# Performance work log

Measured on AMD Instinct MI355X. Metric: run time of the kernel, lower is better.

The kernel has to match this reference:

```python
import jax, jax.numpy as jnp
import numpy as np

S, B, H, I, E = 512, 2, 1024, 2816, 8  # seq_len, batch, hidden, intermediate, num_local_experts


def setup_inputs() -> dict:
    key = jax.random.key(0)
    ks = jax.random.split(key, 5)
    return {
        "hidden_states": jax.random.normal(ks[0], (S, B, H), dtype=jnp.float32),
        "router_w": jax.random.normal(ks[1], (E, H), dtype=jnp.float32) * 0.02,
        "gate_w": jax.random.normal(ks[2], (E, I, H), dtype=jnp.float32) * 0.02,
        "up_w": jax.random.normal(ks[3], (E, I, H), dtype=jnp.float32) * 0.02,
        "down_w": jax.random.normal(ks[4], (E, H, I), dtype=jnp.float32) * 0.02,
    }


def reference(hidden_states, router_w, gate_w, up_w, down_w):
    # Router: linear hidden -> num_experts, top-1 routing (num_experts_per_tok == 1).
    router_logits = jnp.einsum('sbh,eh->sbe', hidden_states, router_w)  # [S,B,E]
    routing_indices = jnp.argmax(router_logits, axis=-1)  # [S,B], top-1 == argmax
    # NOTE: the source computes routing_weights = sigmoid(top logit) but never
    # applies it in _combine_expert_outputs; we faithfully omit the scaling.

    out = jnp.zeros_like(hidden_states)
    for e in range(E):  # fixed small expert count; masked dense dispatch/combine
        mask = (routing_indices == e)[..., None]  # [S,B,1]
        xe = jnp.where(mask, hidden_states, 0.0)
        g = jnp.einsum('sbh,ih->sbi', xe, gate_w[e])
        u = jnp.einsum('sbh,ih->sbi', xe, up_w[e])
        ye = jnp.einsum('sbi,hi->sbh', jax.nn.silu(g) * u, down_w[e])
        out = out + jnp.where(mask, ye, 0.0)
    return out
```

## Files before the change

kernel.cpp:

```cpp
#include <hip/hip_runtime.h>
#include <math.h>

constexpr int H_ = 1024;
constexpr int I_ = 2816;
constexpr int E_ = 8;
constexpr int T_ = 1024;

typedef __bf16 bf16x8 __attribute__((ext_vector_type(8)));
typedef float f32x4 __attribute__((ext_vector_type(4)));

__device__ __forceinline__ ushort f2bf(float f) {
    uint32_t u = __float_as_uint(f);
    u += 0x7fff + ((u >> 16) & 1);
    return (ushort)(u >> 16);
}
__device__ __forceinline__ uint pack2(float lo, float hi) {
    return (uint)f2bf(lo) | ((uint)f2bf(hi) << 16);
}
__device__ __forceinline__ bf16x8 cvt8(float4 a, float4 b) {
    union { uint u[4]; bf16x8 v; } r;
    r.u[0] = pack2(a.x, a.y); r.u[1] = pack2(a.z, a.w);
    r.u[2] = pack2(b.x, b.y); r.u[3] = pack2(b.z, b.w);
    return r.v;
}
__device__ __forceinline__ bf16x8 as_bf16x8(uint4 v) {
    union { uint4 u; bf16x8 b; } c; c.u = v; return c.b;
}


__global__ __launch_bounds__(64) void router_kernel(const float* __restrict__ hidden,
                                                    const float* __restrict__ rw,
                                                    int* __restrict__ counts,
                                                    int* __restrict__ tlist,
                                                    ushort* __restrict__ xbf) {
    const int t = blockIdx.x;
    const int lane = threadIdx.x;
    const float* x = hidden + (size_t)t * H_ + lane * 16;
    float4 v[4];
#pragma unroll
    for (int j = 0; j < 4; j++) v[j] = ((const float4*)x)[j];
    uint2* xb = (uint2*)(xbf + (size_t)t * H_ + lane * 16);
#pragma unroll
    for (int j = 0; j < 4; j++) xb[j] = make_uint2(pack2(v[j].x, v[j].y), pack2(v[j].z, v[j].w));
    float acc[E_];
#pragma unroll
    for (int e = 0; e < E_; e++) {
        const float4* r = (const float4*)(rw + e * H_ + lane * 16);
        float a = 0.f;
#pragma unroll
        for (int j = 0; j < 4; j++) {
            float4 rv = r[j];
            a += v[j].x * rv.x + v[j].y * rv.y + v[j].z * rv.z + v[j].w * rv.w;
        }
        acc[e] = a;
    }
#pragma unroll
    for (int e = 0; e < E_; e++) {
#pragma unroll
        for (int off = 32; off >= 1; off >>= 1)
            acc[e] += __shfl_xor(acc[e], off, 64);
    }
    if (lane == 0) {
        int best = 0;
        float bv = acc[0];
#pragma unroll
        for (int e = 1; e < E_; e++) {
            if (acc[e] > bv) { bv = acc[e]; best = e; }
        }
        int pos = atomicAdd(&counts[best], 1);
        tlist[best * T_ + pos] = t;
    }
}

__global__ __launch_bounds__(256, 2) void gateup_kernel(const ushort* __restrict__ xbf,
                                                        const float* __restrict__ gate_w,
                                                        const float* __restrict__ up_w,
                                                        const int* __restrict__ counts,
                                                        const int* __restrict__ tlist,
                                                        ushort* __restrict__ act) {
    const int e  = blockIdx.y;
    const int i0 = blockIdx.x * 32;
    const int cnt = counts[e];
    const int tid = threadIdx.x;
    const int wv = tid >> 6, lane = tid & 63, quad = lane >> 4, l15 = lane & 15;

    __shared__ int toks[256];

    const float* gw0 = gate_w + ((size_t)e * I_ + i0 + l15) * H_ + quad * 8;
    const float* gw1 = gw0 + (size_t)16 * H_;
    const float* uw0 = up_w   + ((size_t)e * I_ + i0 + l15) * H_ + quad * 8;
    const float* uw1 = uw0 + (size_t)16 * H_;

    for (int toff = 0; toff < cnt; toff += 256) {
        __syncthreads();
        { int p = toff + tid; toks[tid] = (p < cnt) ? tlist[e * T_ + p] : -1; }
        __syncthreads();
        if (cnt - toff <= wv * 64) continue;

        int tka[4];
        const ushort* xa[4];
#pragma unroll
        for (int mi = 0; mi < 4; mi++) {
            tka[mi] = toks[wv * 64 + mi * 16 + l15];
            xa[mi] = xbf + (size_t)(tka[mi] < 0 ? 0 : tka[mi]) * H_ + quad * 8;
        }

        f32x4 accg[4][2], accu[4][2];
#pragma unroll
        for (int mi = 0; mi < 4; mi++)
#pragma unroll
            for (int nj = 0; nj < 2; nj++) {
                accg[mi][nj] = (f32x4){0.f, 0.f, 0.f, 0.f};
                accu[mi][nj] = (f32x4){0.f, 0.f, 0.f, 0.f};
            }

        uint4 a0[4], a1[4];
        float4 g0[2][2], g1[2][2], u0[2][2], u1[2][2];

#define GU_LOAD(A, G, U, kk) do {                                                   \
        const int k_ = (kk);                                                        \
        _Pragma("unroll")                                                           \
        for (int mi = 0; mi < 4; mi++)                                              \
            A[mi] = (tka[mi] >= 0) ? *(const uint4*)(xa[mi] + k_)                   \
                                   : make_uint4(0u, 0u, 0u, 0u);                    \
        G[0][0] = *(const float4*)(gw0 + k_); G[0][1] = *(const float4*)(gw0 + k_ + 4); \
        G[1][0] = *(const float4*)(gw1 + k_); G[1][1] = *(const float4*)(gw1 + k_ + 4); \
        U[0][0] = *(const float4*)(uw0 + k_); U[0][1] = *(const float4*)(uw0 + k_ + 4); \
        U[1][0] = *(const float4*)(uw1 + k_); U[1][1] = *(const float4*)(uw1 + k_ + 4); \
    } while (0)

#define GU_MFMA(A, G, U) do {                                                       \
        bf16x8 bg[2], bu[2];                                                        \
        _Pragma("unroll")                                                           \
        for (int nj = 0; nj < 2; nj++) {                                            \
            bg[nj] = cvt8(G[nj][0], G[nj][1]);                                      \
            bu[nj] = cvt8(U[nj][0], U[nj][1]);                                      \
        }                                                                           \
        _Pragma("unroll")                                                           \
        for (int mi = 0; mi < 4; mi++) {                                            \
            bf16x8 aa = as_bf16x8(A[mi]);                                           \
            _Pragma("unroll")                                                       \
            for (int nj = 0; nj < 2; nj++) {                                        \
                accg[mi][nj] = __builtin_amdgcn_mfma_f32_16x16x32_bf16(aa, bg[nj], accg[mi][nj], 0, 0, 0); \
                accu[mi][nj] = __builtin_amdgcn_mfma_f32_16x16x32_bf16(aa, bu[nj], accu[mi][nj], 0, 0, 0); \
            }                                                                       \
        }                                                                           \
    } while (0)

        GU_LOAD(a0, g0, u0, 0);
#pragma unroll 1
        for (int k0 = 0; k0 < H_; k0 += 64) {
            GU_LOAD(a1, g1, u1, k0 + 32);
            GU_MFMA(a0, g0, u0);
            if (k0 + 64 < H_) GU_LOAD(a0, g0, u0, k0 + 64);
            GU_MFMA(a1, g1, u1);
        }
#undef GU_LOAD
#undef GU_MFMA

#pragma unroll
        for (int mi = 0; mi < 4; mi++)
#pragma unroll
            for (int r = 0; r < 4; r++) {
                int tok = toks[wv * 64 + mi * 16 + quad * 4 + r];
                if (tok < 0) continue;
#pragma unroll
                for (int nj = 0; nj < 2; nj++) {
                    float g = accg[mi][nj][r], u = accu[mi][nj][r];
                    float s = g / (1.f + __expf(-g)) * u;
                    act[(size_t)tok * I_ + i0 + nj * 16 + l15] = f2bf(s);
                }
            }
    }
}

__global__ __launch_bounds__(256, 2) void down_kernel(const ushort* __restrict__ act,
                                                      const float* __restrict__ down_w,
                                                      const int* __restrict__ counts,
                                                      const int* __restrict__ tlist,
                                                      float* __restrict__ out) {
    const int e  = blockIdx.y;
    const int h0 = blockIdx.x * 16;
    const int cnt = counts[e];
    const int tid = threadIdx.x;
    const int wv = tid >> 6, lane = tid & 63, quad = lane >> 4, l15 = lane & 15;

    __shared__ int toks[256];
    const float* dw = down_w + ((size_t)e * H_ + h0 + l15) * I_ + quad * 8;

    for (int toff = 0; toff < cnt; toff += 256) {
        __syncthreads();
        { int p = toff + tid; toks[tid] = (p < cnt) ? tlist[e * T_ + p] : -1; }
        __syncthreads();
        if (cnt - toff <= wv * 64) continue;

        int tka[4];
        const ushort* xa[4];
#pragma unroll
        for (int mi = 0; mi < 4; mi++) {
            tka[mi] = toks[wv * 64 + mi * 16 + l15];
            xa[mi] = act + (size_t)(tka[mi] < 0 ? 0 : tka[mi]) * I_ + quad * 8;
        }

        f32x4 acc[4];
#pragma unroll
        for (int mi = 0; mi < 4; mi++) acc[mi] = (f32x4){0.f, 0.f, 0.f, 0.f};

        uint4 a0[4], a1[4];
        float4 d0[2], d1[2];

#define DN_LOAD(A, D, kk) do {                                                      \
        const int k_ = (kk);                                                        \
        _Pragma("unroll")                                                           \
        for (int mi = 0; mi < 4; mi++)                                              \
            A[mi] = (tka[mi] >= 0) ? *(const uint4*)(xa[mi] + k_)                   \
                                   : make_uint4(0u, 0u, 0u, 0u);                    \
        D[0] = *(const float4*)(dw + k_); D[1] = *(const float4*)(dw + k_ + 4);     \
    } while (0)

#define DN_MFMA(A, D) do {                                                          \
        bf16x8 bd = cvt8(D[0], D[1]);                                               \
        _Pragma("unroll")                                                           \
        for (int mi = 0; mi < 4; mi++) {                                            \
            bf16x8 aa = as_bf16x8(A[mi]);                                           \
            acc[mi] = __builtin_amdgcn_mfma_f32_16x16x32_bf16(aa, bd, acc[mi], 0, 0, 0); \
        }                                                                           \
    } while (0)

        DN_LOAD(a0, d0, 0);
#pragma unroll 1
        for (int k0 = 0; k0 < I_; k0 += 64) {
            DN_LOAD(a1, d1, k0 + 32);
            DN_MFMA(a0, d0);
            if (k0 + 64 < I_) DN_LOAD(a0, d0, k0 + 64);
            DN_MFMA(a1, d1);
        }
#undef DN_LOAD
#undef DN_MFMA

#pragma unroll
        for (int mi = 0; mi < 4; mi++)
#pragma unroll
            for (int r = 0; r < 4; r++) {
                int tok = toks[wv * 64 + mi * 16 + quad * 4 + r];
                if (tok < 0) continue;
                out[(size_t)tok * H_ + h0 + l15] = acc[mi][r];
            }
    }
}

extern "C" void kernel_launch(void* const* d_in, const int* in_sizes, int n_in,
                              void* d_out, int out_size, void* d_ws, size_t ws_size,
                              hipStream_t stream) {
    const float* hidden = (const float*)d_in[0];
    const float* rw     = (const float*)d_in[1];
    const float* gate_w = (const float*)d_in[2];
    const float* up_w   = (const float*)d_in[3];
    const float* down_w = (const float*)d_in[4];
    float* out = (float*)d_out;

    int* counts = (int*)d_ws;
    int* tlist  = counts + E_;
    ushort* xbf = (ushort*)(tlist + E_ * T_);
    ushort* act = xbf + (size_t)T_ * H_;

    hipMemsetAsync(counts, 0, E_ * sizeof(int), stream);
    hipLaunchKernelGGL(router_kernel, dim3(T_), dim3(64), 0, stream, hidden, rw, counts, tlist, xbf);
    hipLaunchKernelGGL(gateup_kernel, dim3(I_ / 32, E_), dim3(256), 0, stream,
                       xbf, gate_w, up_w, counts, tlist, act);
    hipLaunchKernelGGL(down_kernel, dim3(H_ / 16, E_), dim3(256), 0, stream,
                       act, down_w, counts, tlist, out);
}
```

Baseline: 423.1 us.

## Stage gate/up and down operands through LDS with async global-to-LDS copies

Both the gate/up and down kernels now stream activations and weights into swizzled shared memory using global_load_lds async copies. The gate/up kernel double-buffers and the down kernel triple-buffers, with manual vmcnt waits and barriers in place of per-wave register prefetch from global memory. The fp32 weight tile is loaded once per block and shared across the four waves instead of each wave loading it separately, and gateup occupancy is raised to 3 blocks. The cost is extra LDS use, a barrier on every k-step, and hand-tuned wait counts that must match the number of issued copies. Waves with no tokens no longer skip the main loop, so they do redundant work.

```diff
diff --git a/kernel.cpp b/kernel.cpp
--- a/kernel.cpp
+++ b/kernel.cpp
@@ -23,8 +23,23 @@
     r.u[2] = pack2(b.x, b.y); r.u[3] = pack2(b.z, b.w);
     return r.v;
 }
-__device__ __forceinline__ bf16x8 as_bf16x8(uint4 v) {
-    union { uint4 u; bf16x8 b; } c; c.u = v; return c.b;
+
+__device__ __forceinline__ void async_copy16(void* lds, const void* g) {
+    __builtin_amdgcn_global_load_lds(
+        (const __attribute__((address_space(1))) void*)g,
+        (__attribute__((address_space(3))) void*)lds, 16, 0, 0);
+}
+
+__device__ __forceinline__ bf16x8 ldsA(const ushort* base, int row, int quad) {
+    int bir = (quad * 16) ^ (((row >> 1) & 3) << 4);
+    return *(const bf16x8*)((const char*)base + row * 64 + bir);
+}
+__device__ __forceinline__ bf16x8 ldsB(const float* base, int row, int quad) {
+    int sw = (row & 7) << 4;
+    const char* r = (const char*)base + row * 128;
+    float4 x = *(const float4*)(r + ((quad * 32) ^ sw));
+    float4 y = *(const float4*)(r + ((quad * 32 + 16) ^ sw));
+    return cvt8(x, y);
 }
 
 
@@ -72,7 +87,7 @@
     }
 }
 
-__global__ __launch_bounds__(256, 2) void gateup_kernel(const ushort* __restrict__ xbf,
+__global__ __launch_bounds__(256, 3) void gateup_kernel(const ushort* __restrict__ xbf,
                                                         const float* __restrict__ gate_w,
                                                         const float* __restrict__ up_w,
                                                         const int* __restrict__ counts,
@@ -84,25 +99,29 @@
     const int tid = threadIdx.x;
     const int wv = tid >> 6, lane = tid & 63, quad = lane >> 4, l15 = lane & 15;
 
+    __shared__ ushort Xs[2 * 256 * 32];
+    __shared__ float  Gs[2 * 32 * 32];
+    __shared__ float  Us[2 * 32 * 32];
     __shared__ int toks[256];
 
-    const float* gw0 = gate_w + ((size_t)e * I_ + i0 + l15) * H_ + quad * 8;
-    const float* gw1 = gw0 + (size_t)16 * H_;
-    const float* uw0 = up_w   + ((size_t)e * I_ + i0 + l15) * H_ + quad * 8;
-    const float* uw1 = uw0 + (size_t)16 * H_;
+    const int wrow = tid >> 3;
+    const int wbir = ((tid & 7) << 4) ^ ((wrow & 7) << 4);
+    const float* gsrc = gate_w + ((size_t)e * I_ + i0 + wrow) * H_ + (wbir >> 2);
+    const float* usrc = up_w   + ((size_t)e * I_ + i0 + wrow) * H_ + (wbir >> 2);
 
     for (int toff = 0; toff < cnt; toff += 256) {
         __syncthreads();
         { int p = toff + tid; toks[tid] = (p < cnt) ? tlist[e * T_ + p] : -1; }
         __syncthreads();
-        if (cnt - toff <= wv * 64) continue;
-
-        int tka[4];
-        const ushort* xa[4];
-#pragma unroll
-        for (int mi = 0; mi < 4; mi++) {
-            tka[mi] = toks[wv * 64 + mi * 16 + l15];
-            xa[mi] = xbf + (size_t)(tka[mi] < 0 ? 0 : tka[mi]) * H_ + quad * 8;
+
+        const ushort* xsrc[4];
+#pragma unroll
+        for (int p = 0; p < 4; p++) {
+            int row = p * 64 + (tid >> 2);
+            int tok = toks[row];
+            if (tok < 0) tok = 0;
+            int birl = ((tid & 3) << 4) ^ (((row >> 1) & 3) << 4);
+            xsrc[p] = xbf + (size_t)tok * H_ + (birl >> 1);
         }
 
         f32x4 accg[4][2], accu[4][2];
@@ -114,49 +133,53 @@
                 accu[mi][nj] = (f32x4){0.f, 0.f, 0.f, 0.f};
             }
 
-        uint4 a0[4], a1[4];
-        float4 g0[2][2], g1[2][2], u0[2][2], u1[2][2];
-
-#define GU_LOAD(A, G, U, kk) do {                                                   \
-        const int k_ = (kk);                                                        \
-        _Pragma("unroll")                                                           \
-        for (int mi = 0; mi < 4; mi++)                                              \
-            A[mi] = (tka[mi] >= 0) ? *(const uint4*)(xa[mi] + k_)                   \
-                                   : make_uint4(0u, 0u, 0u, 0u);                    \
-        G[0][0] = *(const float4*)(gw0 + k_); G[0][1] = *(const float4*)(gw0 + k_ + 4); \
-        G[1][0] = *(const float4*)(gw1 + k_); G[1][1] = *(const float4*)(gw1 + k_ + 4); \
-        U[0][0] = *(const float4*)(uw0 + k_); U[0][1] = *(const float4*)(uw0 + k_ + 4); \
-        U[1][0] = *(const float4*)(uw1 + k_); U[1][1] = *(const float4*)(uw1 + k_ + 4); \
+#define GSTAGE(buf, kofs) do {                                                  \
+        char* xb_ = (char*)Xs + (buf) * 16384 + wv * 1024;                      \
+        _Pragma("unroll")                                                       \
+        for (int p = 0; p < 4; p++)                                             \
+            async_copy16(xb_ + p * 4096, xsrc[p] + (kofs));                     \
+        async_copy16((char*)Gs + (buf) * 4096 + wv * 1024, gsrc + (kofs));      \
+        async_copy16((char*)Us + (buf) * 4096 + wv * 1024, usrc + (kofs));      \
     } while (0)
 
-#define GU_MFMA(A, G, U) do {                                                       \
-        bf16x8 bg[2], bu[2];                                                        \
-        _Pragma("unroll")                                                           \
-        for (int nj = 0; nj < 2; nj++) {                                            \
-            bg[nj] = cvt8(G[nj][0], G[nj][1]);                                      \
-            bu[nj] = cvt8(U[nj][0], U[nj][1]);                                      \
-        }                                                                           \
-        _Pragma("unroll")                                                           \
-        for (int mi = 0; mi < 4; mi++) {                                            \
-            bf16x8 aa = as_bf16x8(A[mi]);                                           \
-            _Pragma("unroll")                                                       \
-            for (int nj = 0; nj < 2; nj++) {                                        \
-                accg[mi][nj] = __builtin_amdgcn_mfma_f32_16x16x32_bf16(aa, bg[nj], accg[mi][nj], 0, 0, 0); \
-                accu[mi][nj] = __builtin_amdgcn_mfma_f32_16x16x32_bf16(aa, bu[nj], accu[mi][nj], 0, 0, 0); \
-            }                                                                       \
-        }                                                                           \
-    } while (0)
-
-        GU_LOAD(a0, g0, u0, 0);
+        GSTAGE(0, 0);
+        int cur = 0;
 #pragma unroll 1
-        for (int k0 = 0; k0 < H_; k0 += 64) {
-            GU_LOAD(a1, g1, u1, k0 + 32);
-            GU_MFMA(a0, g0, u0);
-            if (k0 + 64 < H_) GU_LOAD(a0, g0, u0, k0 + 64);
-            GU_MFMA(a1, g1, u1);
-        }
-#undef GU_LOAD
-#undef GU_MFMA
+        for (int k0 = 0; k0 < H_; k0 += 32) {
+            if (k0 + 32 < H_) {
+                GSTAGE(cur ^ 1, k0 + 32);
+                asm volatile("s_waitcnt vmcnt(6)" ::: "memory");
+            } else {
+                asm volatile("s_waitcnt vmcnt(0)" ::: "memory");
+            }
+            __builtin_amdgcn_s_barrier();
+            __builtin_amdgcn_sched_barrier(0);
+
+            const ushort* Xb = Xs + cur * 8192;
+            const float*  Gb = Gs + cur * 1024;
+            const float*  Ub = Us + cur * 1024;
+            bf16x8 a[4], bg[2], bu[2];
+#pragma unroll
+            for (int nj = 0; nj < 2; nj++) {
+                bg[nj] = ldsB(Gb, nj * 16 + l15, quad);
+                bu[nj] = ldsB(Ub, nj * 16 + l15, quad);
+            }
+#pragma unroll
+            for (int mi = 0; mi < 4; mi++)
+                a[mi] = ldsA(Xb, wv * 64 + mi * 16 + l15, quad);
+#pragma unroll
+            for (int mi = 0; mi < 4; mi++)
+#pragma unroll
+                for (int nj = 0; nj < 2; nj++) {
+                    accg[mi][nj] = __builtin_amdgcn_mfma_f32_16x16x32_bf16(a[mi], bg[nj], accg[mi][nj], 0, 0, 0);
+                    accu[mi][nj] = __builtin_amdgcn_mfma_f32_16x16x32_bf16(a[mi], bu[nj], accu[mi][nj], 0, 0, 0);
+                }
+            __builtin_amdgcn_sched_barrier(0);
+            __builtin_amdgcn_s_barrier();
+            __builtin_amdgcn_sched_barrier(0);
+            cur ^= 1;
+        }
+#undef GSTAGE
 
 #pragma unroll
         for (int mi = 0; mi < 4; mi++)
@@ -185,58 +208,78 @@
     const int tid = threadIdx.x;
     const int wv = tid >> 6, lane = tid & 63, quad = lane >> 4, l15 = lane & 15;
 
+    __shared__ ushort As[3 * 256 * 32];
+    __shared__ float  Ds[3 * 16 * 32];
     __shared__ int toks[256];
-    const float* dw = down_w + ((size_t)e * H_ + h0 + l15) * I_ + quad * 8;
+
+    const int wrow = (tid >> 3) & 15;
+    const int wbir = ((tid & 7) << 4) ^ ((wrow & 7) << 4);
+    const float* dsrc = down_w + ((size_t)e * H_ + h0 + wrow) * I_ + (wbir >> 2);
 
     for (int toff = 0; toff < cnt; toff += 256) {
         __syncthreads();
         { int p = toff + tid; toks[tid] = (p < cnt) ? tlist[e * T_ + p] : -1; }
         __syncthreads();
-        if (cnt - toff <= wv * 64) continue;
-
-        int tka[4];
-        const ushort* xa[4];
-#pragma unroll
-        for (int mi = 0; mi < 4; mi++) {
-            tka[mi] = toks[wv * 64 + mi * 16 + l15];
-            xa[mi] = act + (size_t)(tka[mi] < 0 ? 0 : tka[mi]) * I_ + quad * 8;
+
+        const ushort* asrc[4];
+#pragma unroll
+        for (int p = 0; p < 4; p++) {
+            int row = p * 64 + (tid >> 2);
+            int tok = toks[row];
+            if (tok < 0) tok = 0;
+            int birl = ((tid & 3) << 4) ^ (((row >> 1) & 3) << 4);
+            asrc[p] = act + (size_t)tok * I_ + (birl >> 1);
         }
 
         f32x4 acc[4];
 #pragma unroll
         for (int mi = 0; mi < 4; mi++) acc[mi] = (f32x4){0.f, 0.f, 0.f, 0.f};
 
-        uint4 a0[4], a1[4];
-        float4 d0[2], d1[2];
-
-#define DN_LOAD(A, D, kk) do {                                                      \
-        const int k_ = (kk);                                                        \
-        _Pragma("unroll")                                                           \
-        for (int mi = 0; mi < 4; mi++)                                              \
-            A[mi] = (tka[mi] >= 0) ? *(const uint4*)(xa[mi] + k_)                   \
-                                   : make_uint4(0u, 0u, 0u, 0u);                    \
-        D[0] = *(const float4*)(dw + k_); D[1] = *(const float4*)(dw + k_ + 4);     \
+#define DSTAGE(buf, kofs) do {                                                  \
+        char* ab_ = (char*)As + (buf) * 16384 + wv * 1024;                      \
+        _Pragma("unroll")                                                       \
+        for (int p = 0; p < 4; p++)                                             \
+            async_copy16(ab_ + p * 4096, asrc[p] + (kofs));                     \
+        if (wv < 2)                                                             \
+            async_copy16((char*)Ds + (buf) * 2048 + wv * 1024, dsrc + (kofs));  \
     } while (0)
 
-#define DN_MFMA(A, D) do {                                                          \
-        bf16x8 bd = cvt8(D[0], D[1]);                                               \
-        _Pragma("unroll")                                                           \
-        for (int mi = 0; mi < 4; mi++) {                                            \
-            bf16x8 aa = as_bf16x8(A[mi]);                                           \
-            acc[mi] = __builtin_amdgcn_mfma_f32_16x16x32_bf16(aa, bd, acc[mi], 0, 0, 0); \
-        }                                                                           \
-    } while (0)
-
-        DN_LOAD(a0, d0, 0);
+        DSTAGE(0, 0);
+        DSTAGE(1, 32);
+        int cur = 0;
 #pragma unroll 1
-        for (int k0 = 0; k0 < I_; k0 += 64) {
-            DN_LOAD(a1, d1, k0 + 32);
-            DN_MFMA(a0, d0);
-            if (k0 + 64 < I_) DN_LOAD(a0, d0, k0 + 64);
-            DN_MFMA(a1, d1);
-        }
-#undef DN_LOAD
-#undef DN_MFMA
+        for (int k0 = 0; k0 < I_; k0 += 32) {
+            if (k0 + 64 < I_) {
+                int stg = cur ? cur - 1 : 2;
+                DSTAGE(stg, k0 + 64);
+                if (wv < 2) asm volatile("s_waitcnt vmcnt(10)" ::: "memory");
+                else        asm volatile("s_waitcnt vmcnt(8)"  ::: "memory");
+            } else if (k0 + 32 < I_) {
+                if (wv < 2) asm volatile("s_waitcnt vmcnt(5)" ::: "memory");
+                else        asm volatile("s_waitcnt vmcnt(4)" ::: "memory");
+            } else {
+                asm volatile("s_waitcnt vmcnt(0)" ::: "memory");
+            }
+            __builtin_amdgcn_s_barrier();
+            __builtin_amdgcn_sched_barrier(0);
+
+            const ushort* Ab = As + cur * 8192;
+            const float*  Db = Ds + cur * 512;
+            bf16x8 a[4];
+            bf16x8 bd = ldsB(Db, l15, quad);
+#pragma unroll
+            for (int mi = 0; mi < 4; mi++)
+                a[mi] = ldsA(Ab, wv * 64 + mi * 16 + l15, quad);
+#pragma unroll
+            for (int mi = 0; mi < 4; mi++)
+                acc[mi] = __builtin_amdgcn_mfma_f32_16x16x32_bf16(a[mi], bd, acc[mi], 0, 0, 0);
+
+            __builtin_amdgcn_sched_barrier(0);
+            __builtin_amdgcn_s_barrier();
+            __builtin_amdgcn_sched_barrier(0);
+            cur = (cur == 2) ? 0 : cur + 1;
+        }
+#undef DSTAGE
 
 #pragma unroll
         for (int mi = 0; mi < 4; mi++)
```

Measured after the change: 382.9 us. 1.1x faster.

## Stage expert weights into LDS with async global_load_lds and swizzled multi-buffering

Applied to the files above, without the earlier changes.

Both expert GEMM kernels now stream fp32 weight tiles into a 4-deep swizzled LDS ring using global_load_lds, with manual vmcnt waits and barriers. Previously each wave loaded the weights straight into registers. Sharing the staged tiles across the four waves removes redundant global weight loads, and the XOR swizzle avoids LDS bank conflicts. The patch also switches to the hardware packed bf16 convert, interleaves experts across a 1D grid, and raises gateup occupancy to 3. The tradeoffs are hand-tuned waitcnt counts that are fragile and the removal of early exit for idle waves, since all waves must now join the barriers.

```diff
diff --git a/kernel.cpp b/kernel.cpp
--- a/kernel.cpp
+++ b/kernel.cpp
@@ -17,14 +17,22 @@
 __device__ __forceinline__ uint pack2(float lo, float hi) {
     return (uint)f2bf(lo) | ((uint)f2bf(hi) << 16);
 }
-__device__ __forceinline__ bf16x8 cvt8(float4 a, float4 b) {
-    union { uint u[4]; bf16x8 v; } r;
-    r.u[0] = pack2(a.x, a.y); r.u[1] = pack2(a.z, a.w);
-    r.u[2] = pack2(b.x, b.y); r.u[3] = pack2(b.z, b.w);
-    return r.v;
-}
 __device__ __forceinline__ bf16x8 as_bf16x8(uint4 v) {
     union { uint4 u; bf16x8 b; } c; c.u = v; return c.b;
+}
+__device__ __forceinline__ bf16x8 cvt8pk(float4 a, float4 b) {
+    union { uint u[4]; bf16x8 v; } r;
+    asm("v_cvt_pk_bf16_f32 %0, %1, %2" : "=v"(r.u[0]) : "v"(a.x), "v"(a.y));
+    asm("v_cvt_pk_bf16_f32 %0, %1, %2" : "=v"(r.u[1]) : "v"(a.z), "v"(a.w));
+    asm("v_cvt_pk_bf16_f32 %0, %1, %2" : "=v"(r.u[2]) : "v"(b.x), "v"(b.y));
+    asm("v_cvt_pk_bf16_f32 %0, %1, %2" : "=v"(r.u[3]) : "v"(b.z), "v"(b.w));
+    return r.v;
+}
+
+__device__ __forceinline__ void async_copy16(void* lds, const void* g) {
+    __builtin_amdgcn_global_load_lds(
+        (const __attribute__((address_space(1))) void*)g,
+        (__attribute__((address_space(3))) void*)lds, 16, 0, 0);
 }
 
 
@@ -72,33 +80,41 @@
     }
 }
 
-__global__ __launch_bounds__(256, 2) void gateup_kernel(const ushort* __restrict__ xbf,
+__global__ __launch_bounds__(256, 3) void gateup_kernel(const ushort* __restrict__ xbf,
                                                         const float* __restrict__ gate_w,
                                                         const float* __restrict__ up_w,
                                                         const int* __restrict__ counts,
                                                         const int* __restrict__ tlist,
                                                         ushort* __restrict__ act) {
-    const int e  = blockIdx.y;
-    const int i0 = blockIdx.x * 32;
+    const int id = blockIdx.x;
+    const int e  = id & 7;
+    const int i0 = (id >> 3) * 32;
     const int cnt = counts[e];
     const int tid = threadIdx.x;
     const int wv = tid >> 6, lane = tid & 63, quad = lane >> 4, l15 = lane & 15;
 
+    __shared__ float Gs[4 * 1024];
+    __shared__ float Us[4 * 1024];
     __shared__ int toks[256];
 
-    const float* gw0 = gate_w + ((size_t)e * I_ + i0 + l15) * H_ + quad * 8;
-    const float* gw1 = gw0 + (size_t)16 * H_;
-    const float* uw0 = up_w   + ((size_t)e * I_ + i0 + l15) * H_ + quad * 8;
-    const float* uw1 = uw0 + (size_t)16 * H_;
+    const int wrow = tid >> 3;
+    const int wcol = (((tid & 7) ^ (wrow & 7)) << 2);
+    const float* gsrc = gate_w + ((size_t)e * I_ + i0 + wrow) * H_ + wcol;
+    const float* usrc = up_w   + ((size_t)e * I_ + i0 + wrow) * H_ + wcol;
+    char* gdst = (char*)Gs + wv * 1024;
+    char* udst = (char*)Us + wv * 1024;
+
+#define STAGEW(buf, kofs) do {                                                  \
+        async_copy16(gdst + (buf) * 4096, gsrc + (kofs));                       \
+        async_copy16(udst + (buf) * 4096, usrc + (kofs));                       \
+    } while (0)
 
     for (int toff = 0; toff < cnt; toff += 256) {
         __syncthreads();
         { int p = toff + tid; toks[tid] = (p < cnt) ? tlist[e * T_ + p] : -1; }
         __syncthreads();
-        if (cnt - toff <= wv * 64) continue;
-
-        int tka[4];
-        const ushort* xa[4];
+
+        int tka[4]; const ushort* xa[4];
 #pragma unroll
         for (int mi = 0; mi < 4; mi++) {
             tka[mi] = toks[wv * 64 + mi * 16 + l15];
@@ -114,49 +130,60 @@
                 accu[mi][nj] = (f32x4){0.f, 0.f, 0.f, 0.f};
             }
 
-        uint4 a0[4], a1[4];
-        float4 g0[2][2], g1[2][2], u0[2][2], u1[2][2];
-
-#define GU_LOAD(A, G, U, kk) do {                                                   \
-        const int k_ = (kk);                                                        \
-        _Pragma("unroll")                                                           \
-        for (int mi = 0; mi < 4; mi++)                                              \
-            A[mi] = (tka[mi] >= 0) ? *(const uint4*)(xa[mi] + k_)                   \
-                                   : make_uint4(0u, 0u, 0u, 0u);                    \
-        G[0][0] = *(const float4*)(gw0 + k_); G[0][1] = *(const float4*)(gw0 + k_ + 4); \
-        G[1][0] = *(const float4*)(gw1 + k_); G[1][1] = *(const float4*)(gw1 + k_ + 4); \
-        U[0][0] = *(const float4*)(uw0 + k_); U[0][1] = *(const float4*)(uw0 + k_ + 4); \
-        U[1][0] = *(const float4*)(uw1 + k_); U[1][1] = *(const float4*)(uw1 + k_ + 4); \
-    } while (0)
-
-#define GU_MFMA(A, G, U) do {                                                       \
-        bf16x8 bg[2], bu[2];                                                        \
-        _Pragma("unroll")                                                           \
-        for (int nj = 0; nj < 2; nj++) {                                            \
-            bg[nj] = cvt8(G[nj][0], G[nj][1]);                                      \
-            bu[nj] = cvt8(U[nj][0], U[nj][1]);                                      \
-        }                                                                           \
-        _Pragma("unroll")                                                           \
-        for (int mi = 0; mi < 4; mi++) {                                            \
-            bf16x8 aa = as_bf16x8(A[mi]);                                           \
-            _Pragma("unroll")                                                       \
-            for (int nj = 0; nj < 2; nj++) {                                        \
+        uint4 xc[4], xn[4];
+        STAGEW(0, 0);
+        STAGEW(1, 32);
+#pragma unroll
+        for (int mi = 0; mi < 4; mi++) xc[mi] = *(const uint4*)(xa[mi]);
+
+#define GBODY(k, XU, XL) do {                                                   \
+        const int t_ = (k) >> 5;                                                \
+        if ((k) + 32 < H_) {                                                    \
+            _Pragma("unroll")                                                   \
+            for (int mi = 0; mi < 4; mi++)                                      \
+                XL[mi] = *(const uint4*)(xa[mi] + (k) + 32);                    \
+        }                                                                       \
+        __builtin_amdgcn_sched_barrier(0);                                      \
+        if ((k) + 64 < H_) {                                                    \
+            STAGEW((t_ + 2) & 3, (k) + 64);                                     \
+            __builtin_amdgcn_sched_barrier(0);                                  \
+            asm volatile("s_waitcnt vmcnt(12)" ::: "memory");                   \
+        } else {                                                                \
+            asm volatile("s_waitcnt vmcnt(0)" ::: "memory");                    \
+        }                                                                       \
+        __builtin_amdgcn_s_barrier();                                           \
+        __builtin_amdgcn_sched_barrier(0);                                      \
+        const float* Gb = Gs + (t_ & 3) * 1024;                                 \
+        const float* Ub = Us + (t_ & 3) * 1024;                                 \
+        bf16x8 bg[2], bu[2];                                                    \
+        const int sw_ = (l15 & 7) << 4;                                         \
+        _Pragma("unroll")                                                       \
+        for (int nj = 0; nj < 2; nj++) {                                        \
+            const char* gr = (const char*)Gb + (nj * 16 + l15) * 128;           \
+            const char* ur = (const char*)Ub + (nj * 16 + l15) * 128;           \
+            bg[nj] = cvt8pk(*(const float4*)(gr + ((quad * 32) ^ sw_)),         \
+                            *(const float4*)(gr + ((quad * 32 + 16) ^ sw_)));   \
+            bu[nj] = cvt8pk(*(const float4*)(ur + ((quad * 32) ^ sw_)),         \
+                            *(const float4*)(ur + ((quad * 32 + 16) ^ sw_)));   \
+        }                                                                       \
+        _Pragma("unroll")                                                       \
+        for (int mi = 0; mi < 4; mi++) {                                        \
+            bf16x8 aa = as_bf16x8(XU[mi]);                                      \
+            _Pragma("unroll")                                                   \
+            for (int nj = 0; nj < 2; nj++) {                                    \
                 accg[mi][nj] = __builtin_amdgcn_mfma_f32_16x16x32_bf16(aa, bg[nj], accg[mi][nj], 0, 0, 0); \
                 accu[mi][nj] = __builtin_amdgcn_mfma_f32_16x16x32_bf16(aa, bu[nj], accu[mi][nj], 0, 0, 0); \
-            }                                                                       \
-        }                                                                           \
+            }                                                                   \
+        }                                                                       \
+        __builtin_amdgcn_sched_barrier(0);                                      \
     } while (0)
 
-        GU_LOAD(a0, g0, u0, 0);
 #pragma unroll 1
         for (int k0 = 0; k0 < H_; k0 += 64) {
-            GU_LOAD(a1, g1, u1, k0 + 32);
-            GU_MFMA(a0, g0, u0);
-            if (k0 + 64 < H_) GU_LOAD(a0, g0, u0, k0 + 64);
-            GU_MFMA(a1, g1, u1);
-        }
-#undef GU_LOAD
-#undef GU_MFMA
+            GBODY(k0, xc, xn);
+            GBODY(k0 + 32, xn, xc);
+        }
+#undef GBODY
 
 #pragma unroll
         for (int mi = 0; mi < 4; mi++)
@@ -172,6 +199,7 @@
                 }
             }
     }
+#undef STAGEW
 }
 
 __global__ __launch_bounds__(256, 2) void down_kernel(const ushort* __restrict__ act,
@@ -179,23 +207,29 @@
                                                       const int* __restrict__ counts,
                                                       const int* __restrict__ tlist,
                                                       float* __restrict__ out) {
-    const int e  = blockIdx.y;
-    const int h0 = blockIdx.x * 16;
+    const int id = blockIdx.x;
+    const int e  = id & 7;
+    const int h0 = (id >> 3) * 16;
     const int cnt = counts[e];
     const int tid = threadIdx.x;
     const int wv = tid >> 6, lane = tid & 63, quad = lane >> 4, l15 = lane & 15;
 
+    __shared__ float Ws[4 * 1024];
     __shared__ int toks[256];
-    const float* dw = down_w + ((size_t)e * H_ + h0 + l15) * I_ + quad * 8;
+
+    const int wrow = tid >> 4;
+    const int wcol = (((tid & 15) ^ (wrow & 7)) << 2);
+    const float* dsrc = down_w + ((size_t)e * H_ + h0 + wrow) * I_ + wcol;
+    char* ddst = (char*)Ws + wv * 1024;
+
+#define STAGED(buf, kofs) async_copy16(ddst + (buf) * 4096, dsrc + (kofs))
 
     for (int toff = 0; toff < cnt; toff += 256) {
         __syncthreads();
         { int p = toff + tid; toks[tid] = (p < cnt) ? tlist[e * T_ + p] : -1; }
         __syncthreads();
-        if (cnt - toff <= wv * 64) continue;
-
-        int tka[4];
-        const ushort* xa[4];
+
+        int tka[4]; const ushort* xa[4];
 #pragma unroll
         for (int mi = 0; mi < 4; mi++) {
             tka[mi] = toks[wv * 64 + mi * 16 + l15];
@@ -206,37 +240,55 @@
 #pragma unroll
         for (int mi = 0; mi < 4; mi++) acc[mi] = (f32x4){0.f, 0.f, 0.f, 0.f};
 
-        uint4 a0[4], a1[4];
-        float4 d0[2], d1[2];
-
-#define DN_LOAD(A, D, kk) do {                                                      \
-        const int k_ = (kk);                                                        \
-        _Pragma("unroll")                                                           \
-        for (int mi = 0; mi < 4; mi++)                                              \
-            A[mi] = (tka[mi] >= 0) ? *(const uint4*)(xa[mi] + k_)                   \
-                                   : make_uint4(0u, 0u, 0u, 0u);                    \
-        D[0] = *(const float4*)(dw + k_); D[1] = *(const float4*)(dw + k_ + 4);     \
+        uint4 ac[8], an[8];
+        STAGED(0, 0);
+        STAGED(1, 64);
+#pragma unroll
+        for (int mi = 0; mi < 4; mi++) {
+            ac[mi * 2 + 0] = *(const uint4*)(xa[mi]);
+            ac[mi * 2 + 1] = *(const uint4*)(xa[mi] + 32);
+        }
+
+#define DBODY(k, AU, AL) do {                                                   \
+        const int t_ = (k) >> 6;                                                \
+        if ((k) + 64 < I_) {                                                    \
+            _Pragma("unroll")                                                   \
+            for (int mi = 0; mi < 4; mi++) {                                    \
+                AL[mi * 2 + 0] = *(const uint4*)(xa[mi] + (k) + 64);            \
+                AL[mi * 2 + 1] = *(const uint4*)(xa[mi] + (k) + 96);            \
+            }                                                                   \
+        }                                                                       \
+        __builtin_amdgcn_sched_barrier(0);                                      \
+        if ((k) + 128 < I_) {                                                   \
+            STAGED((t_ + 2) & 3, (k) + 128);                                    \
+            __builtin_amdgcn_sched_barrier(0);                                  \
+            asm volatile("s_waitcnt vmcnt(18)" ::: "memory");                   \
+        } else {                                                                \
+            asm volatile("s_waitcnt vmcnt(0)" ::: "memory");                    \
+        }                                                                       \
+        __builtin_amdgcn_s_barrier();                                           \
+        __builtin_amdgcn_sched_barrier(0);                                      \
+        const char* Wb = (const char*)(Ws + (t_ & 3) * 1024) + l15 * 256;       \
+        const int sw_ = (l15 & 7) << 4;                                         \
+        _Pragma("unroll")                                                       \
+        for (int h = 0; h < 2; h++) {                                           \
+            bf16x8 bd = cvt8pk(                                                 \
+                *(const float4*)(Wb + ((h * 128 + quad * 32) ^ sw_)),           \
+                *(const float4*)(Wb + ((h * 128 + quad * 32 + 16) ^ sw_)));     \
+            _Pragma("unroll")                                                   \
+            for (int mi = 0; mi < 4; mi++)                                      \
+                acc[mi] = __builtin_amdgcn_mfma_f32_16x16x32_bf16(              \
+                    as_bf16x8(AU[mi * 2 + h]), bd, acc[mi], 0, 0, 0);           \
+        }                                                                       \
+        __builtin_amdgcn_sched_barrier(0);                                      \
     } while (0)
 
-#define DN_MFMA(A, D) do {                                                          \
-        bf16x8 bd = cvt8(D[0], D[1]);                                               \
-        _Pragma("unroll")                                                           \
-        for (int mi = 0; mi < 4; mi++) {                                            \
-            bf16x8 aa = as_bf16x8(A[mi]);                                           \
-            acc[mi] = __builtin_amdgcn_mfma_f32_16x16x32_bf16(aa, bd, acc[mi], 0, 0, 0); \
-        }                                                                           \
-    } while (0)
-
-        DN_LOAD(a0, d0, 0);
 #pragma unroll 1
-        for (int k0 = 0; k0 < I_; k0 += 64) {
-            DN_LOAD(a1, d1, k0 + 32);
-            DN_MFMA(a0, d0);
-            if (k0 + 64 < I_) DN_LOAD(a0, d0, k0 + 64);
-            DN_MFMA(a1, d1);
-        }
-#undef DN_LOAD
-#undef DN_MFMA
+        for (int k0 = 0; k0 < I_; k0 += 128) {
+            DBODY(k0, ac, an);
+            DBODY(k0 + 64, an, ac);
+        }
+#undef DBODY
 
 #pragma unroll
         for (int mi = 0; mi < 4; mi++)
@@ -247,6 +299,7 @@
                 out[(size_t)tok * H_ + h0 + l15] = acc[mi][r];
             }
     }
+#undef STAGED
 }
 
 extern "C" void kernel_launch(void* const* d_in, const int* in_sizes, int n_in,
@@ -266,8 +319,8 @@
 
     hipMemsetAsync(counts, 0, E_ * sizeof(int), stream);
     hipLaunchKernelGGL(router_kernel, dim3(T_), dim3(64), 0, stream, hidden, rw, counts, tlist, xbf);
-    hipLaunchKernelGGL(gateup_kernel, dim3(I_ / 32, E_), dim3(256), 0, stream,
+    hipLaunchKernelGGL(gateup_kernel, dim3((I_ / 32) * E_), dim3(256), 0, stream,
                        xbf, gate_w, up_w, counts, tlist, act);
-    hipLaunchKernelGGL(down_kernel, dim3(H_ / 16, E_), dim3(256), 0, stream,
+    hipLaunchKernelGGL(down_kernel, dim3((H_ / 16) * E_), dim3(256), 0, stream,
                        act, down_w, counts, tlist, out);
 }
```

Measured after the change: 371.1 us. -12.3%, faster.
